# Kernel tuning notes

Measured on AMD Instinct MI355X. Metric: run time of the kernel, lower is better.

The kernel has to match this reference:

```python
import jax, jax.numpy as jnp
import numpy as np

DIM = 768
NUM_HEADS = 12
HEAD_DIM = DIM // NUM_HEADS


def setup_inputs() -> dict:
    key = jax.random.key(0)
    k1, k2, k3 = jax.random.split(key, 3)
    B, N, C = 8, 4096, DIM
    x = jax.random.normal(k1, (B, N, C), dtype=jnp.float32)
    # torch nn.Linear weights are (out_features, in_features)
    W_qkv = jax.random.normal(k2, (3 * C, C), dtype=jnp.float32) * 0.02
    b_qkv = jnp.zeros((3 * C,), dtype=jnp.float32)
    W_proj = jax.random.normal(k3, (C, C), dtype=jnp.float32) * 0.02
    b_proj = jnp.zeros((C,), dtype=jnp.float32)
    return {"x": x, "W_qkv": W_qkv, "b_qkv": b_qkv, "W_proj": W_proj, "b_proj": b_proj}


def reference(x, W_qkv, b_qkv, W_proj, b_proj):
    B, N, C = x.shape
    H, D = NUM_HEADS, HEAD_DIM
    # qkv projection -> (3, B, H, N, D)
    qkv = (x @ W_qkv.T + b_qkv).reshape(B, N, 3, H, D).transpose(2, 0, 3, 1, 4)
    q, k, v = qkv[0], qkv[1], qkv[2]
    # feature map: elu(x) + 1 (positive kernel features)
    q = jax.nn.elu(q) + 1.0
    k = jax.nn.elu(k) + 1.0
    # kernelized linear attention: (K^T V) then Q (K^T V)
    kv = jnp.einsum('bhnd,bhnv->bhdv', k, v)          # (B,H,D,D)
    out = jnp.einsum('bhnd,bhdv->bhnv', q, kv)        # (B,H,N,D)
    k_sum = k.sum(axis=2)                             # (B,H,D)
    normalizer = jnp.einsum('bhnd,bhd->bhn', q, k_sum) + 1e-06
    out = out / normalizer[..., None]
    out = out.transpose(0, 2, 1, 3).reshape(B, N, C)
    out = out @ W_proj.T + b_proj
    return out
```

## Files before the change

### kernel.cpp

```cpp
#include <hip/hip_runtime.h>
#include <hip/hip_fp16.h>
#include <math.h>

#define NHEADS 12
#define SEQ 4096
#define BATCH 8

typedef _Float16 half8 __attribute__((ext_vector_type(8)));
typedef float floatx4 __attribute__((ext_vector_type(4)));

__global__ void zero_kernel(float* p, int n) {
  int i = blockIdx.x * 256 + threadIdx.x;
  if (i < n) p[i] = 0.f;
}

__global__ void cast_f2h(const float* __restrict__ in, __half* __restrict__ out, int n) {
  int i = (blockIdx.x * 256 + threadIdx.x) * 4;
  if (i < n) {
    float4 v = *(const float4*)&in[i];
    ushort4 o;
    o.x = __half_as_ushort(__float2half(v.x));
    o.y = __half_as_ushort(__float2half(v.y));
    o.z = __half_as_ushort(__float2half(v.z));
    o.w = __half_as_ushort(__float2half(v.w));
    *(ushort4*)&out[i] = o;
  }
}

__device__ __forceinline__ void gld16(const __half* g, _Float16* dst) {
  __builtin_amdgcn_global_load_lds((const __attribute__((address_space(1))) void*)g,
                                   (__attribute__((address_space(3))) void*)dst, 16, 0, 0);
}

__device__ __forceinline__ int fragoff(int row, int quad) {
  const int mp = row >> 1;
  const int p  = ((row & 1) << 2) | quad;
  return (mp * 8 + (p ^ (mp & 7))) * 8;
}

__device__ __forceinline__ void write_l64(_Float16* lds, int row, int col, float v) {
  lds[row * 64 + ((((col >> 3) ^ (row & 7))) << 3) + (col & 7)] = (_Float16)v;
}
__device__ __forceinline__ half8 read_l64c(const _Float16* lds, int row, int c) {
  return *(const half8*)(lds + row * 64 + ((c ^ (row & 7)) << 3));
}

__device__ __forceinline__ void barrier_raw() {
  asm volatile("s_barrier" ::: "memory");
}

__global__ __launch_bounds__(512, 2) void hgemm_kv8_kernel(
    const __half* __restrict__ A, const __half* __restrict__ W,
    const float* __restrict__ bias,
    __half* __restrict__ outK, __half* __restrict__ outV)
{
  const int K = 768;
  const int NT = 24;
  extern __shared__ __align__(16) _Float16 sh[];
  const int t    = threadIdx.x;
  const int w    = t >> 6;
  const int l    = t & 63;
  const int quad = l >> 4;
  const int mrow = l & 15;
  const int wm   = w >> 2;
  const int wn   = w & 3;

  const int bid  = blockIdx.x;
  const int xcd  = bid & 7;
  const int ii   = bid >> 3;
  const int mg   = ii / 6;
  const int jj   = ii - mg * 6;
  const int m0   = (xcd * 16 + mg) * 256;
  const int j0   = jj * 256;

  const int mp  = t >> 3;
  const int pp  = (t & 7) ^ (mp & 7);
  const int rsw = mp * 2 + (pp >> 2);
  const int qsw = (pp & 3) * 8;
  const __half* gA0 = A + (size_t)(m0 + rsw) * K + qsw;
  const __half* gA1 = gA0 + (size_t)128 * K;
  const __half* gW0 = W + (size_t)(768 + j0 + rsw) * K + qsw;
  const __half* gW1 = gW0 + (size_t)128 * K;
  const int ld = (t >> 6) * 512;

  int aoff[8], boff[4];
#pragma unroll
  for (int i = 0; i < 8; ++i)
    aoff[i] = wm * 4096 + fragoff(i * 16 + mrow, quad);
#pragma unroll
  for (int j = 0; j < 4; ++j) {
    const int C = wn * 64 + j * 16 + mrow;
    boff[j] = 8192 + (C >> 7) * 4096 + fragoff(C & 127, quad);
  }

  floatx4 acc[8][4];
#pragma unroll
  for (int i = 0; i < 8; ++i)
#pragma unroll
    for (int j = 0; j < 4; ++j) acc[i][j] = (floatx4){0.f, 0.f, 0.f, 0.f};

#pragma unroll
  for (int kt = 0; kt < 3; ++kt) {
    _Float16* db = sh + kt * 16384;
    const int kg = kt * 32;
    gld16(gA0 + kg, db + ld);
    gld16(gA1 + kg, db + 4096 + ld);
    gld16(gW0 + kg, db + 8192 + ld);
    gld16(gW1 + kg, db + 12288 + ld);
  }
  asm volatile("s_waitcnt vmcnt(8)" ::: "memory");
  barrier_raw();

#pragma unroll 4
  for (int kt = 0; kt < NT; ++kt) {
    const _Float16* bb = sh + (kt & 3) * 16384;
    const bool st = (kt + 3 < NT);
    _Float16* db = sh + ((kt + 3) & 3) * 16384;
    const int kg = (kt + 3) * 32;
    half8 af[4], bf[4];

#pragma unroll
    for (int j = 0; j < 4; ++j) bf[j] = *(const half8*)(bb + boff[j]);
#pragma unroll
    for (int i = 0; i < 4; ++i) af[i] = *(const half8*)(bb + aoff[i]);
    if (st) {
      gld16(gA0 + kg, db + ld);
      gld16(gA1 + kg, db + 4096 + ld);
    }
    barrier_raw();
    __builtin_amdgcn_s_setprio(1);
#pragma unroll
    for (int i = 0; i < 4; ++i)
#pragma unroll
      for (int j = 0; j < 4; ++j)
        acc[i][j] = __builtin_amdgcn_mfma_f32_16x16x32_f16(af[i], bf[j], acc[i][j], 0, 0, 0);
    __builtin_amdgcn_s_setprio(0);

#pragma unroll
    for (int i = 0; i < 4; ++i) af[i] = *(const half8*)(bb + aoff[i + 4]);
    if (st) {
      gld16(gW0 + kg, db + 8192 + ld);
      gld16(gW1 + kg, db + 12288 + ld);
    }
    barrier_raw();
    __builtin_amdgcn_s_setprio(1);
#pragma unroll
    for (int i = 0; i < 4; ++i)
#pragma unroll
      for (int j = 0; j < 4; ++j)
        acc[i + 4][j] = __builtin_amdgcn_mfma_f32_16x16x32_f16(af[i], bf[j], acc[i + 4][j], 0, 0, 0);
    __builtin_amdgcn_s_setprio(0);

    if (kt < NT - 3)       asm volatile("s_waitcnt vmcnt(8)" ::: "memory");
    else if (kt == NT - 3) asm volatile("s_waitcnt vmcnt(4)" ::: "memory");
    else if (kt == NT - 2) asm volatile("s_waitcnt vmcnt(0)" ::: "memory");
    barrier_raw();
  }

  const int col0 = 768 + j0 + wn * 64;
  const int t3   = col0 / 768;
  const int h    = (col0 - t3 * 768) >> 6;
  __half* dst    = (t3 == 1) ? outK : outV;
  const int m0w  = m0 + wm * 128;
  const int b_   = m0w >> 12;
  const int n0w  = m0w & 4095;
  _Float16* scr  = sh + w * 4096;
  const size_t gbT = (size_t)(b_ * NHEADS + h) * 64 * 4096;

#pragma unroll
  for (int hf = 0; hf < 2; ++hf) {
#pragma unroll
    for (int j = 0; j < 4; ++j) {
      const int col = j * 16 + mrow;
      const float bsv = bias[col0 + col];
#pragma unroll
      for (int ii2 = 0; ii2 < 4; ++ii2)
#pragma unroll
        for (int r = 0; r < 4; ++r) {
          const int row = ii2 * 16 + quad * 4 + r;
          float val = acc[hf * 4 + ii2][j][r] + bsv;
          if (t3 == 1) val = (val > 0.f) ? (val + 1.f) : expf(val);
          write_l64(scr, col, row, val);
        }
    }
    barrier_raw();
#pragma unroll
    for (int it = 0; it < 8; ++it) {
      const int dd = it * 8 + (l >> 3);
      const int c  = l & 7;
      half8 vv = read_l64c(scr, dd, c);
      *(half8*)((_Float16*)dst + gbT + (size_t)dd * 4096 + n0w + hf * 64 + c * 8) = vv;
    }
    barrier_raw();
  }
}

__global__ __launch_bounds__(256, 3) void hgemm_proj_kernel(
    const __half* __restrict__ A, const __half* __restrict__ W,
    const float* __restrict__ bias, float* __restrict__ outF)
{
  const int K = 768;
  const int NT = 24;
  __shared__ __align__(16) _Float16 sh[3 * 8192];
  const int t    = threadIdx.x;
  const int w    = t >> 6;
  const int l    = t & 63;
  const int quad = l >> 4;
  const int mrow = l & 15;
  const int wr   = (w >> 1) * 64;
  const int wc   = (w & 1) * 64;

  const int bid  = blockIdx.x;
  const int xcd  = bid & 7;
  const int ii   = bid >> 3;
  const int mg   = ii / 6;
  const int jj   = ii - mg * 6;
  const int m0   = (xcd * 32 + mg) * 128;
  const int j0   = jj * 128;

  const int s1  = 256 + t;
  const int mpa = t >> 3,  ppa = (t & 7) ^ (mpa & 7);
  const int ra  = mpa * 2 + (ppa >> 2), qa = (ppa & 3) * 8;
  const int mpb = s1 >> 3, ppb = (s1 & 7) ^ (mpb & 7);
  const int rb  = mpb * 2 + (ppb >> 2), qb = (ppb & 3) * 8;
  const int lda_ = (t >> 6) * 512;
  const int ldb_ = (s1 >> 6) * 512;
  const __half* gA_0 = A + (size_t)(m0 + ra) * K + qa;
  const __half* gA_1 = A + (size_t)(m0 + rb) * K + qb;
  const __half* gB_0 = W + (size_t)(j0 + ra) * K + qa;
  const __half* gB_1 = W + (size_t)(j0 + rb) * K + qb;

  int aoff[4], boff[4];
#pragma unroll
  for (int i = 0; i < 4; ++i) aoff[i] = fragoff(wr + i * 16 + mrow, quad);
#pragma unroll
  for (int j = 0; j < 4; ++j) boff[j] = 4096 + fragoff(wc + j * 16 + mrow, quad);

  floatx4 acc[4][4];
#pragma unroll
  for (int i = 0; i < 4; ++i)
#pragma unroll
    for (int j = 0; j < 4; ++j) acc[i][j] = (floatx4){0.f, 0.f, 0.f, 0.f};

  gld16(gA_0, sh + lda_);           gld16(gA_1, sh + ldb_);
  gld16(gB_0, sh + 4096 + lda_);    gld16(gB_1, sh + 4096 + ldb_);
  gld16(gA_0 + 32, sh + 8192 + lda_);        gld16(gA_1 + 32, sh + 8192 + ldb_);
  gld16(gB_0 + 32, sh + 12288 + lda_);       gld16(gB_1 + 32, sh + 12288 + ldb_);
  asm volatile("s_waitcnt vmcnt(4)" ::: "memory");
  barrier_raw();

  int cur = 0, nxt = 2;
#pragma unroll 3
  for (int kt = 0; kt < NT; ++kt) {
    const _Float16* bb = sh + cur * 8192;
    _Float16* db = sh + nxt * 8192;
    const bool st = (kt + 2 < NT);
    const int kg = (kt + 2) * 32;

    if (st) {
      gld16(gA_0 + kg, db + lda_);        gld16(gA_1 + kg, db + ldb_);
      gld16(gB_0 + kg, db + 4096 + lda_); gld16(gB_1 + kg, db + 4096 + ldb_);
    }
    half8 af[4], bf[4];
#pragma unroll
    for (int i = 0; i < 4; ++i) af[i] = *(const half8*)(bb + aoff[i]);
#pragma unroll
    for (int j = 0; j < 4; ++j) bf[j] = *(const half8*)(bb + boff[j]);
#pragma unroll
    for (int i = 0; i < 4; ++i)
#pragma unroll
      for (int j = 0; j < 4; ++j)
        acc[i][j] = __builtin_amdgcn_mfma_f32_16x16x32_f16(af[i], bf[j], acc[i][j], 0, 0, 0);

    if (kt < NT - 2)       asm volatile("s_waitcnt vmcnt(4)" ::: "memory");
    else if (kt == NT - 2) asm volatile("s_waitcnt vmcnt(0)" ::: "memory");
    barrier_raw();
    cur = (cur + 1) % 3;
    nxt = (nxt + 1) % 3;
  }

#pragma unroll
  for (int j = 0; j < 4; ++j) {
    const int col = j0 + wc + j * 16 + mrow;
    const float bsv = bias[col];
#pragma unroll
    for (int i = 0; i < 4; ++i)
#pragma unroll
      for (int r = 0; r < 4; ++r) {
        const int m = m0 + wr + i * 16 + quad * 4 + r;
        outF[(size_t)m * 768 + col] = acc[i][j][r] + bsv;
      }
  }
}

__global__ __launch_bounds__(256) void kv_mfma_kernel(
    const __half* __restrict__ kT, const __half* __restrict__ vT,
    float* __restrict__ kv, float* __restrict__ ksum)
{
  extern __shared__ float red[];
  float* ksr = red + 4 * 4096;
  const int bh = blockIdx.x;
  const int sp = blockIdx.y;
  const int t  = threadIdx.x;
  const int w  = t >> 6;
  const int l  = t & 63;
  const int quad = l >> 4;
  const int mrow = l & 15;
  const size_t base = (size_t)bh * 64 * 4096;
  const int n0 = sp * 1024 + w * 256;

  floatx4 acc[4][4];
  floatx4 ks[4];
#pragma unroll
  for (int i = 0; i < 4; ++i) {
    ks[i] = (floatx4){0.f, 0.f, 0.f, 0.f};
#pragma unroll
    for (int j = 0; j < 4; ++j) acc[i][j] = (floatx4){0.f, 0.f, 0.f, 0.f};
  }
  half8 ones;
#pragma unroll
  for (int e = 0; e < 8; ++e) ones[e] = (_Float16)1.0f;

  const __half* pk[4];
  const __half* pv[4];
#pragma unroll
  for (int i = 0; i < 4; ++i) {
    pk[i] = kT + base + (size_t)(i * 16 + mrow) * 4096 + n0 + quad * 8;
    pv[i] = vT + base + (size_t)(i * 16 + mrow) * 4096 + n0 + quad * 8;
  }

#pragma unroll
  for (int nn = 0; nn < 256; nn += 32) {
    half8 af[4], bf[4];
#pragma unroll
    for (int i = 0; i < 4; ++i) af[i] = *(const half8*)(pk[i] + nn);
#pragma unroll
    for (int j = 0; j < 4; ++j) bf[j] = *(const half8*)(pv[j] + nn);
#pragma unroll
    for (int i = 0; i < 4; ++i)
#pragma unroll
      for (int j = 0; j < 4; ++j)
        acc[i][j] = __builtin_amdgcn_mfma_f32_16x16x32_f16(af[i], bf[j], acc[i][j], 0, 0, 0);
#pragma unroll
    for (int i = 0; i < 4; ++i)
      ks[i] = __builtin_amdgcn_mfma_f32_16x16x32_f16(af[i], ones, ks[i], 0, 0, 0);
  }

  float* rw = red + w * 4096;
#pragma unroll
  for (int i = 0; i < 4; ++i)
#pragma unroll
    for (int j = 0; j < 4; ++j)
#pragma unroll
      for (int r = 0; r < 4; ++r)
        rw[(i * 16 + quad * 4 + r) * 64 + j * 16 + mrow] = acc[i][j][r];
  if (mrow == 0) {
#pragma unroll
    for (int i = 0; i < 4; ++i)
#pragma unroll
      for (int r = 0; r < 4; ++r)
        ksr[w * 64 + i * 16 + quad * 4 + r] = ks[i][r];
  }
  __syncthreads();
#pragma unroll
  for (int ii = 0; ii < 16; ++ii) {
    const int idx = ii * 256 + t;
    const float s = red[idx] + red[4096 + idx] + red[8192 + idx] + red[12288 + idx];
    atomicAdd(&kv[(size_t)bh * 4096 + idx], s);
  }
  if (t < 64)
    atomicAdd(&ksum[(size_t)bh * 64 + t], ksr[t] + ksr[64 + t] + ksr[128 + t] + ksr[192 + t]);
}

__global__ __launch_bounds__(256) void qattn_kernel(
    const __half* __restrict__ A, const __half* __restrict__ W,
    const float* __restrict__ bias,
    const float* __restrict__ kvg, const float* __restrict__ ksumg,
    __half* __restrict__ att)
{
  const int K = 768;
  const int NT = 24;
  __shared__ __align__(16) _Float16 sh[24576];
  __shared__ float norms[256];
  __shared__ float ksums[128];
  const int t    = threadIdx.x;
  const int w    = t >> 6;
  const int l    = t & 63;
  const int quad = l >> 4;
  const int mrow = l & 15;
  const int m0   = blockIdx.x * 128;
  const int j0   = blockIdx.y * 128;
  const int wr   = (w >> 1) * 64;
  const int wc   = (w & 1) * 64;
  const int b_   = m0 >> 12;
  const int h0   = j0 >> 6;

  {
    _Float16* kvT0 = sh + 16384;
#pragma unroll
    for (int ii = 0; ii < 32; ++ii) {
      const int gidx = ii * 256 + t;
      const int head = gidx >> 12;
      const int r    = gidx & 4095;
      const float val = kvg[(size_t)(b_ * NHEADS + h0 + head) * 4096 + r];
      write_l64(kvT0 + head * 4096, r & 63, r >> 6, val);
    }
    if (t < 128) ksums[t] = ksumg[(size_t)(b_ * NHEADS + h0 + (t >> 6)) * 64 + (t & 63)];
  }

  const int s1  = 256 + t;
  const int mpa = t >> 3,  ppa = (t & 7) ^ (mpa & 7);
  const int ra  = mpa * 2 + (ppa >> 2), qa = (ppa & 3) * 8;
  const int mpb = s1 >> 3, ppb = (s1 & 7) ^ (mpb & 7);
  const int rb  = mpb * 2 + (ppb >> 2), qb = (ppb & 3) * 8;
  const int lda_ = (t >> 6) * 512;
  const int ldb_ = (s1 >> 6) * 512;
  const __half* gA_0 = A + (size_t)(m0 + ra) * K + qa;
  const __half* gA_1 = A + (size_t)(m0 + rb) * K + qb;
  const __half* gB_0 = W + (size_t)(j0 + ra) * K + qa;
  const __half* gB_1 = W + (size_t)(j0 + rb) * K + qb;

  int aoff[4], boff[4];
#pragma unroll
  for (int i = 0; i < 4; ++i) aoff[i] = fragoff(wr + i * 16 + mrow, quad);
#pragma unroll
  for (int j = 0; j < 4; ++j) boff[j] = 4096 + fragoff(wc + j * 16 + mrow, quad);

  floatx4 acc[4][4];
#pragma unroll
  for (int i = 0; i < 4; ++i)
#pragma unroll
    for (int j = 0; j < 4; ++j) acc[i][j] = (floatx4){0.f, 0.f, 0.f, 0.f};

  gld16(gA_0, sh + lda_);         gld16(gA_1, sh + ldb_);
  gld16(gB_0, sh + 4096 + lda_);  gld16(gB_1, sh + 4096 + ldb_);
  asm volatile("s_waitcnt vmcnt(0)" ::: "memory");
  barrier_raw();

#pragma unroll 2
  for (int kt = 0; kt < NT; ++kt) {
    const _Float16* bb = sh + (kt & 1) * 8192;
    _Float16* db = sh + ((kt + 1) & 1) * 8192;
    const bool st = (kt + 1 < NT);
    const int kg = (kt + 1) * 32;

    if (st) {
      gld16(gA_0 + kg, db + lda_);        gld16(gA_1 + kg, db + ldb_);
      gld16(gB_0 + kg, db + 4096 + lda_); gld16(gB_1 + kg, db + 4096 + ldb_);
    }
    half8 af[4], bf[4];
#pragma unroll
    for (int i = 0; i < 4; ++i) af[i] = *(const half8*)(bb + aoff[i]);
#pragma unroll
    for (int j = 0; j < 4; ++j) bf[j] = *(const half8*)(bb + boff[j]);
#pragma unroll
    for (int i = 0; i < 4; ++i)
#pragma unroll
      for (int j = 0; j < 4; ++j)
        acc[i][j] = __builtin_amdgcn_mfma_f32_16x16x32_f16(af[i], bf[j], acc[i][j], 0, 0, 0);

    if (st) asm volatile("s_waitcnt vmcnt(0)" ::: "memory");
    barrier_raw();
  }

  _Float16* qtile = sh + w * 4096;
  const _Float16* kvT = sh + 16384 + (w & 1) * 4096;
  const int hh = w & 1;

  __syncthreads();
#pragma unroll
  for (int j = 0; j < 4; ++j) {
    const int col = j * 16 + mrow;
    const float bsv = bias[j0 + wc + col];
#pragma unroll
    for (int i = 0; i < 4; ++i)
#pragma unroll
      for (int r = 0; r < 4; ++r) {
        const int row = i * 16 + quad * 4 + r;
        float val = acc[i][j][r] + bsv;
        val = (val > 0.f) ? (val + 1.f) : expf(val);
        write_l64(qtile, row, col, val);
      }
  }
  __syncthreads();

  {
    float nrm = 0.f;
#pragma unroll
    for (int c = 0; c < 8; ++c) {
      half8 qv = read_l64c(qtile, l, c);
#pragma unroll
      for (int e = 0; e < 8; ++e) nrm += (float)qv[e] * ksums[hh * 64 + c * 8 + e];
    }
    norms[w * 64 + l] = 1.f / (nrm + 1e-6f);
  }

  floatx4 oacc[4][4];
#pragma unroll
  for (int i = 0; i < 4; ++i)
#pragma unroll
    for (int j = 0; j < 4; ++j) oacc[i][j] = (floatx4){0.f, 0.f, 0.f, 0.f};
#pragma unroll
  for (int ks = 0; ks < 2; ++ks) {
    half8 af[4], bf[4];
#pragma unroll
    for (int i = 0; i < 4; ++i) af[i] = read_l64c(qtile, i * 16 + mrow, ks * 4 + quad);
#pragma unroll
    for (int j = 0; j < 4; ++j) bf[j] = read_l64c(kvT, j * 16 + mrow, ks * 4 + quad);
#pragma unroll
    for (int i = 0; i < 4; ++i)
#pragma unroll
      for (int j = 0; j < 4; ++j)
        oacc[i][j] = __builtin_amdgcn_mfma_f32_16x16x32_f16(af[i], bf[j], oacc[i][j], 0, 0, 0);
  }
  __syncthreads();

#pragma unroll
  for (int i = 0; i < 4; ++i)
#pragma unroll
    for (int r = 0; r < 4; ++r) {
      const int row = i * 16 + quad * 4 + r;
      const float rn = norms[w * 64 + row];
#pragma unroll
      for (int j = 0; j < 4; ++j)
        write_l64(qtile, row, j * 16 + mrow, oacc[i][j][r] * rn);
    }
  __syncthreads();
  const int n0w = (m0 & 4095) + wr;
  const size_t abase = (size_t)(b_ * SEQ + n0w) * 768 + (h0 + hh) * 64;
#pragma unroll
  for (int it = 0; it < 8; ++it) {
    const int row = it * 8 + (l >> 3);
    const int c   = l & 7;
    half8 vv = read_l64c(qtile, row, c);
    *(half8*)((_Float16*)att + abase + (size_t)row * 768 + c * 8) = vv;
  }
}

extern "C" void kernel_launch(void* const* d_in, const int* in_sizes, int n_in,
                              void* d_out, int out_size, void* d_ws, size_t ws_size,
                              hipStream_t stream)
{
  const float* x     = (const float*)d_in[0];
  const float* Wqkv  = (const float*)d_in[1];
  const float* bqkv  = (const float*)d_in[2];
  const float* Wproj = (const float*)d_in[3];
  const float* bproj = (const float*)d_in[4];
  float* out = (float*)d_out;

  const size_t SZ = (size_t)BATCH * NHEADS * SEQ * 64;
  __half* xh  = (__half*)d_ws;
  __half* Wqh = xh + SZ;
  __half* Wph = Wqh + (size_t)2304 * 768;
  __half* R3  = Wph + (size_t)768 * 768;
  __half* R4  = R3 + SZ;
  float*  kvb = (float*)(R4 + SZ);
  float*  ksum = kvb + 96 * 64 * 64;

  static bool attr_set = false;
  if (!attr_set) {
    hipFuncSetAttribute((const void*)hgemm_kv8_kernel,
                        hipFuncAttributeMaxDynamicSharedMemorySize, 131072);
    hipFuncSetAttribute((const void*)kv_mfma_kernel,
                        hipFuncAttributeMaxDynamicSharedMemorySize, 66560);
    attr_set = true;
  }

  zero_kernel<<<1560, 256, 0, stream>>>(kvb, 96 * 64 * 64 + 96 * 64);

  cast_f2h<<<(int)(SZ / 1024), 256, 0, stream>>>(x, xh, (int)SZ);
  cast_f2h<<<(2304 * 768) / 1024, 256, 0, stream>>>(Wqkv, Wqh, 2304 * 768);
  cast_f2h<<<(768 * 768) / 1024, 256, 0, stream>>>(Wproj, Wph, 768 * 768);

  hgemm_kv8_kernel<<<768, 512, 131072, stream>>>(xh, Wqh, bqkv, R3, R4);

  kv_mfma_kernel<<<dim3(96, 4), 256, 66560, stream>>>(R3, R4, kvb, ksum);

  qattn_kernel<<<dim3(256, 6), 256, 0, stream>>>(
      xh, Wqh, bqkv, kvb, ksum, R3);

  hgemm_proj_kernel<<<1536, 256, 0, stream>>>(R3, Wph, bproj, out);
}
```

Baseline: 447.2 us.

## Restructure qattn kernel to 256-row tiles with 4-stage LDS pipeline and XCD swizzle

The fused Q-projection/attention kernel now runs 512 threads per block on a 256x128 output tile. It uses a 4-buffer global-to-LDS pipeline with three tiles in flight, and maps block IDs so blocks on the same XCD share rows of x. Block-wide __syncthreads in the epilogue are replaced by per-wave lgkmcnt waits, since each wave touches only its own qtile region. The intent is to hide load latency, reuse the W tile across more rows, and improve L2 locality. The cost is more LDS per block (dynamic 112KB) and fewer resident blocks per CU.

```diff
diff --git a/kernel.cpp b/kernel.cpp
--- a/kernel.cpp
+++ b/kernel.cpp
@@ -36,6 +36,21 @@
   const int mp = row >> 1;
   const int p  = ((row & 1) << 2) | quad;
   return (mp * 8 + (p ^ (mp & 7))) * 8;
+}
+
+__device__ __forceinline__ void stage_tile(const __half* __restrict__ gbase, int ldg,
+                                           _Float16* lds, int t) {
+#pragma unroll
+  for (int it = 0; it < 2; ++it) {
+    const int s  = it * 256 + t;
+    const int mp = s >> 3, ps = s & 7;
+    const int p  = ps ^ (mp & 7);
+    const int r  = mp * 2 + (p >> 2);
+    const int q  = p & 3;
+    const __half* g = gbase + (size_t)r * ldg + q * 8;
+    _Float16* dst = lds + (s >> 6) * 512;
+    gld16(g, dst);
+  }
 }
 
 __device__ __forceinline__ void write_l64(_Float16* lds, int row, int col, float v) {
@@ -372,7 +387,7 @@
     atomicAdd(&ksum[(size_t)bh * 64 + t], ksr[t] + ksr[64 + t] + ksr[128 + t] + ksr[192 + t]);
 }
 
-__global__ __launch_bounds__(256) void qattn_kernel(
+__global__ __launch_bounds__(512, 2) void qattn_kernel(
     const __half* __restrict__ A, const __half* __restrict__ W,
     const float* __restrict__ bias,
     const float* __restrict__ kvg, const float* __restrict__ ksumg,
@@ -380,51 +395,57 @@
 {
   const int K = 768;
   const int NT = 24;
-  __shared__ __align__(16) _Float16 sh[24576];
-  __shared__ float norms[256];
+  extern __shared__ __align__(16) _Float16 sh[];
+  __shared__ float norms[512];
   __shared__ float ksums[128];
   const int t    = threadIdx.x;
   const int w    = t >> 6;
   const int l    = t & 63;
   const int quad = l >> 4;
   const int mrow = l & 15;
-  const int m0   = blockIdx.x * 128;
-  const int j0   = blockIdx.y * 128;
   const int wr   = (w >> 1) * 64;
-  const int wc   = (w & 1) * 64;
-  const int b_   = m0 >> 12;
-  const int h0   = j0 >> 6;
-
-  {
-    _Float16* kvT0 = sh + 16384;
-#pragma unroll
-    for (int ii = 0; ii < 32; ++ii) {
-      const int gidx = ii * 256 + t;
-      const int head = gidx >> 12;
-      const int r    = gidx & 4095;
-      const float val = kvg[(size_t)(b_ * NHEADS + h0 + head) * 4096 + r];
-      write_l64(kvT0 + head * 4096, r & 63, r >> 6, val);
-    }
-    if (t < 128) ksums[t] = ksumg[(size_t)(b_ * NHEADS + h0 + (t >> 6)) * 64 + (t & 63)];
-  }
-
-  const int s1  = 256 + t;
-  const int mpa = t >> 3,  ppa = (t & 7) ^ (mpa & 7);
-  const int ra  = mpa * 2 + (ppa >> 2), qa = (ppa & 3) * 8;
-  const int mpb = s1 >> 3, ppb = (s1 & 7) ^ (mpb & 7);
-  const int rb  = mpb * 2 + (ppb >> 2), qb = (ppb & 3) * 8;
-  const int lda_ = (t >> 6) * 512;
-  const int ldb_ = (s1 >> 6) * 512;
-  const __half* gA_0 = A + (size_t)(m0 + ra) * K + qa;
-  const __half* gA_1 = A + (size_t)(m0 + rb) * K + qb;
-  const __half* gB_0 = W + (size_t)(j0 + ra) * K + qa;
-  const __half* gB_1 = W + (size_t)(j0 + rb) * K + qb;
+  const int hh   = w & 1;
+  const int wc   = hh * 64;
+
+  const int bid = blockIdx.x;
+  const int xcd = bid & 7;
+  const int ii  = bid >> 3;
+  const int mg  = ii / 6;
+  const int jj  = ii - mg * 6;
+  const int m0  = (xcd * 16 + mg) * 256;
+  const int j0  = jj * 128;
+  const int b_  = m0 >> 12;
+  const int h0  = jj * 2;
+
+  _Float16* kvT0 = sh + 49152;
+
+#pragma unroll
+  for (int it = 0; it < 16; ++it) {
+    const int gidx = it * 512 + t;
+    const int head = gidx >> 12;
+    const int r    = gidx & 4095;
+    const float val = kvg[(size_t)(b_ * NHEADS + h0 + head) * 4096 + r];
+    write_l64(kvT0 + head * 4096, r & 63, r >> 6, val);
+  }
+  if (t < 128) ksums[t] = ksumg[(size_t)(b_ * NHEADS + h0 + (t >> 6)) * 64 + (t & 63)];
+
+  const int mp  = t >> 3;
+  const int pp  = (t & 7) ^ (mp & 7);
+  const int rsw = mp * 2 + (pp >> 2);
+  const int qsw = (pp & 3) * 8;
+  const __half* gA0 = A + (size_t)(m0 + rsw) * K + qsw;
+  const __half* gA1 = gA0 + (size_t)128 * K;
+  const __half* gB0 = W + (size_t)(j0 + rsw) * K + qsw;
+  const int ld = (t >> 6) * 512;
 
   int aoff[4], boff[4];
 #pragma unroll
-  for (int i = 0; i < 4; ++i) aoff[i] = fragoff(wr + i * 16 + mrow, quad);
-#pragma unroll
-  for (int j = 0; j < 4; ++j) boff[j] = 4096 + fragoff(wc + j * 16 + mrow, quad);
+  for (int i = 0; i < 4; ++i) {
+    const int rowi = wr + i * 16 + mrow;
+    aoff[i] = (rowi >> 7) * 4096 + fragoff(rowi & 127, quad);
+  }
+#pragma unroll
+  for (int j = 0; j < 4; ++j) boff[j] = 8192 + fragoff(wc + j * 16 + mrow, quad);
 
   floatx4 acc[4][4];
 #pragma unroll
@@ -432,42 +453,48 @@
 #pragma unroll
     for (int j = 0; j < 4; ++j) acc[i][j] = (floatx4){0.f, 0.f, 0.f, 0.f};
 
-  gld16(gA_0, sh + lda_);         gld16(gA_1, sh + ldb_);
-  gld16(gB_0, sh + 4096 + lda_);  gld16(gB_1, sh + 4096 + ldb_);
-  asm volatile("s_waitcnt vmcnt(0)" ::: "memory");
+#pragma unroll
+  for (int kt = 0; kt < 3; ++kt) {
+    _Float16* db = sh + kt * 12288;
+    const int kg = kt * 32;
+    gld16(gA0 + kg, db + ld);
+    gld16(gA1 + kg, db + 4096 + ld);
+    gld16(gB0 + kg, db + 8192 + ld);
+  }
+  asm volatile("s_waitcnt vmcnt(6)" ::: "memory");
   barrier_raw();
 
-#pragma unroll 2
+#pragma unroll 4
   for (int kt = 0; kt < NT; ++kt) {
-    const _Float16* bb = sh + (kt & 1) * 8192;
-    _Float16* db = sh + ((kt + 1) & 1) * 8192;
-    const bool st = (kt + 1 < NT);
-    const int kg = (kt + 1) * 32;
-
+    const _Float16* bb = sh + (kt & 3) * 12288;
+    const bool st = (kt + 3 < NT);
+    _Float16* db = sh + ((kt + 3) & 3) * 12288;
+    const int kg = (kt + 3) * 32;
+    half8 af[4], bf[4];
+
+#pragma unroll
+    for (int j = 0; j < 4; ++j) bf[j] = *(const half8*)(bb + boff[j]);
+#pragma unroll
+    for (int i = 0; i < 4; ++i) af[i] = *(const half8*)(bb + aoff[i]);
     if (st) {
-      gld16(gA_0 + kg, db + lda_);        gld16(gA_1 + kg, db + ldb_);
-      gld16(gB_0 + kg, db + 4096 + lda_); gld16(gB_1 + kg, db + 4096 + ldb_);
-    }
-    half8 af[4], bf[4];
-#pragma unroll
-    for (int i = 0; i < 4; ++i) af[i] = *(const half8*)(bb + aoff[i]);
-#pragma unroll
-    for (int j = 0; j < 4; ++j) bf[j] = *(const half8*)(bb + boff[j]);
+      gld16(gA0 + kg, db + ld);
+      gld16(gA1 + kg, db + 4096 + ld);
+      gld16(gB0 + kg, db + 8192 + ld);
+    }
 #pragma unroll
     for (int i = 0; i < 4; ++i)
 #pragma unroll
       for (int j = 0; j < 4; ++j)
         acc[i][j] = __builtin_amdgcn_mfma_f32_16x16x32_f16(af[i], bf[j], acc[i][j], 0, 0, 0);
 
-    if (st) asm volatile("s_waitcnt vmcnt(0)" ::: "memory");
+    if (kt < NT - 3)       asm volatile("s_waitcnt vmcnt(6)" ::: "memory");
+    else if (kt == NT - 3) asm volatile("s_waitcnt vmcnt(3)" ::: "memory");
+    else if (kt == NT - 2) asm volatile("s_waitcnt vmcnt(0)" ::: "memory");
     barrier_raw();
   }
 
   _Float16* qtile = sh + w * 4096;
-  const _Float16* kvT = sh + 16384 + (w & 1) * 4096;
-  const int hh = w & 1;
-
-  __syncthreads();
+
 #pragma unroll
   for (int j = 0; j < 4; ++j) {
     const int col = j * 16 + mrow;
@@ -482,7 +509,8 @@
         write_l64(qtile, row, col, val);
       }
   }
-  __syncthreads();
+  asm volatile("s_waitcnt lgkmcnt(0)" ::: "memory");
+  __builtin_amdgcn_sched_barrier(0);
 
   {
     float nrm = 0.f;
@@ -495,6 +523,7 @@
     norms[w * 64 + l] = 1.f / (nrm + 1e-6f);
   }
 
+  const _Float16* kvT = kvT0 + hh * 4096;
   floatx4 oacc[4][4];
 #pragma unroll
   for (int i = 0; i < 4; ++i)
@@ -502,18 +531,19 @@
     for (int j = 0; j < 4; ++j) oacc[i][j] = (floatx4){0.f, 0.f, 0.f, 0.f};
 #pragma unroll
   for (int ks = 0; ks < 2; ++ks) {
-    half8 af[4], bf[4];
-#pragma unroll
-    for (int i = 0; i < 4; ++i) af[i] = read_l64c(qtile, i * 16 + mrow, ks * 4 + quad);
-#pragma unroll
-    for (int j = 0; j < 4; ++j) bf[j] = read_l64c(kvT, j * 16 + mrow, ks * 4 + quad);
+    half8 af2[4], bf2[4];
+#pragma unroll
+    for (int i = 0; i < 4; ++i) af2[i] = read_l64c(qtile, i * 16 + mrow, ks * 4 + quad);
+#pragma unroll
+    for (int j = 0; j < 4; ++j) bf2[j] = read_l64c(kvT, j * 16 + mrow, ks * 4 + quad);
 #pragma unroll
     for (int i = 0; i < 4; ++i)
 #pragma unroll
       for (int j = 0; j < 4; ++j)
-        oacc[i][j] = __builtin_amdgcn_mfma_f32_16x16x32_f16(af[i], bf[j], oacc[i][j], 0, 0, 0);
-  }
-  __syncthreads();
+        oacc[i][j] = __builtin_amdgcn_mfma_f32_16x16x32_f16(af2[i], bf2[j], oacc[i][j], 0, 0, 0);
+  }
+  asm volatile("s_waitcnt lgkmcnt(0)" ::: "memory");
+  __builtin_amdgcn_sched_barrier(0);
 
 #pragma unroll
   for (int i = 0; i < 4; ++i)
@@ -525,7 +555,9 @@
       for (int j = 0; j < 4; ++j)
         write_l64(qtile, row, j * 16 + mrow, oacc[i][j][r] * rn);
     }
-  __syncthreads();
+  asm volatile("s_waitcnt lgkmcnt(0)" ::: "memory");
+  __builtin_amdgcn_sched_barrier(0);
+
   const int n0w = (m0 & 4095) + wr;
   const size_t abase = (size_t)(b_ * SEQ + n0w) * 768 + (h0 + hh) * 64;
 #pragma unroll
@@ -563,6 +595,8 @@
                         hipFuncAttributeMaxDynamicSharedMemorySize, 131072);
     hipFuncSetAttribute((const void*)kv_mfma_kernel,
                         hipFuncAttributeMaxDynamicSharedMemorySize, 66560);
+    hipFuncSetAttribute((const void*)qattn_kernel,
+                        hipFuncAttributeMaxDynamicSharedMemorySize, 114688);
     attr_set = true;
   }
 
@@ -576,7 +610,7 @@
 
   kv_mfma_kernel<<<dim3(96, 4), 256, 66560, stream>>>(R3, R4, kvb, ksum);
 
-  qattn_kernel<<<dim3(256, 6), 256, 0, stream>>>(
+  qattn_kernel<<<768, 512, 114688, stream>>>(
       xh, Wqh, bqkv, kvb, ksum, R3);
 
   hgemm_proj_kernel<<<1536, 256, 0, stream>>>(R3, Wph, bproj, out);
```

Result: no change. 442.6 us (-1.0%).
